# Kernel optimization log

Measured on AMD Instinct MI355X. Metric: run time of the kernel, lower is better.

Reference implementation:

```python
import jax, jax.numpy as jnp
import numpy as np

N_NODES = 50000
N_EDGES = 800000
HIDDEN = 128


def setup_inputs() -> dict:
    key = jax.random.key(0)
    k_emb, k_ei, k1, k2, k3, kb1, kb2, kb3 = jax.random.split(key, 8)
    emb = jax.random.normal(k_emb, (N_NODES, HIDDEN), dtype=jnp.float32)
    edge_index = jax.random.randint(k_ei, (2, N_EDGES), 0, N_NODES, dtype=jnp.int64)
    h = HIDDEN
    # MLP([2h, 4h, h, 1]) weights, Kaiming-uniform-ish init
    def lin(k, fan_in, fan_out):
        bound = 1.0 / np.sqrt(fan_in)
        return jax.random.uniform(k, (fan_in, fan_out), jnp.float32, -bound, bound)
    W1 = lin(k1, 2 * h, 4 * h)
    b1 = jax.random.uniform(kb1, (4 * h,), jnp.float32, -1.0 / np.sqrt(2 * h), 1.0 / np.sqrt(2 * h))
    W2 = lin(k2, 4 * h, h)
    b2 = jax.random.uniform(kb2, (h,), jnp.float32, -1.0 / np.sqrt(4 * h), 1.0 / np.sqrt(4 * h))
    W3 = lin(k3, h, 1)
    b3 = jax.random.uniform(kb3, (1,), jnp.float32, -1.0 / np.sqrt(h), 1.0 / np.sqrt(h))
    return {"emb": emb, "edge_index": edge_index,
            "W1": W1, "b1": b1, "W2": W2, "b2": b2, "W3": W3, "b3": b3}


def reference(emb, edge_index, W1, b1, W2, b2, W3, b3):
    # learn_edge_att=True path: gather endpoints, concat, 3-layer MLP
    col, row = edge_index[0], edge_index[1]
    f12 = jnp.concatenate([emb[col], emb[row]], axis=-1)  # [E, 2h]
    x = jax.nn.relu(f12 @ W1 + b1)                         # [E, 4h]
    x = jax.nn.relu(x @ W2 + b2)                           # [E, h]
    att_log_logits = x @ W3 + b3                           # [E, 1]
    return att_log_logits
```

## Files before the change

### kernel.cpp

```cpp
#include <hip/hip_runtime.h>
#include <hip/hip_bf16.h>
#include <stdint.h>

#define N_EDGES   800000
#define N_NODESC  50000
#define HID       128

typedef __attribute__((ext_vector_type(8))) short bf16x8;
typedef __attribute__((ext_vector_type(4))) short bf16x4;
typedef __attribute__((ext_vector_type(4))) float f32x4;

__device__ __forceinline__ short f2bf(float f) {
    union { float f; uint32_t u; } v; v.f = f;
    uint32_t r = v.u + 0x7FFFu + ((v.u >> 16) & 1u);
    return (short)(r >> 16);
}
__device__ __forceinline__ float bf2f(short s) {
    union { uint32_t u; float f; } v;
    v.u = ((uint32_t)(uint16_t)s) << 16;
    return v.f;
}

#define PQ_OFF   0UL
#define W1S_OFF  102400000UL
#define W2S_OFF  (W1S_OFF + 262144UL)

__global__ __launch_bounds__(256) void swizzle_kernel(const float* __restrict__ W1,
                                                      const float* __restrict__ W2,
                                                      short* __restrict__ W1s,
                                                      short* __restrict__ W2s) {
    int t = blockIdx.x * 256 + threadIdx.x;
    int lane = t & 63;
    int kq = lane >> 4;
    int nn = lane & 15;
    if (t < 16384) {
        int frag = t >> 6;
        int kc = frag >> 6;
        int nt = frag & 63;
        int n = nt * 16 + nn;
        int kbase = kc * 32 + kq * 8;
        bf16x8 v;
        #pragma unroll
        for (int j = 0; j < 8; ++j) {
            int k = kbase + j;
            float f = (n < 512) ? W1[k * 512 + n] : W1[(128 + k) * 512 + (n - 512)];
            v[j] = f2bf(f);
        }
        *(bf16x8*)(W1s + frag * 512 + lane * 8) = v;
    } else if (t < 24576) {
        int t2 = t - 16384;
        int frag = t2 >> 6;
        int kc = frag >> 3;
        int nt = frag & 7;
        int n = nt * 16 + nn;
        int kbase = kc * 32 + kq * 8;
        bf16x8 v;
        #pragma unroll
        for (int j = 0; j < 8; ++j) v[j] = f2bf(W2[(kbase + j) * HID + n]);
        *(bf16x8*)(W2s + frag * 512 + lane * 8) = v;
    }
}

__global__ __launch_bounds__(256) void precompute_kernel(const float* __restrict__ emb,
                                                         const short* __restrict__ W1s,
                                                         const float* __restrict__ b1,
                                                         short* __restrict__ PQ) {
    int lane = threadIdx.x & 63;
    int w = threadIdx.x >> 6;
    int nb = blockIdx.x * 16;
    int m = lane & 15;
    int kq = lane >> 4;

    f32x4 acc[16];
    #pragma unroll
    for (int i = 0; i < 16; ++i) acc[i] = (f32x4){0.f, 0.f, 0.f, 0.f};

    const float* arow = emb + (size_t)(nb + m) * 128 + kq * 8;
    #pragma unroll
    for (int kc = 0; kc < 4; ++kc) {
        f32x4 a0 = *(const f32x4*)(arow + kc * 32);
        f32x4 a1 = *(const f32x4*)(arow + kc * 32 + 4);
        bf16x8 a;
        a[0] = f2bf(a0[0]); a[1] = f2bf(a0[1]); a[2] = f2bf(a0[2]); a[3] = f2bf(a0[3]);
        a[4] = f2bf(a1[0]); a[5] = f2bf(a1[1]); a[6] = f2bf(a1[2]); a[7] = f2bf(a1[3]);
        #pragma unroll
        for (int nt = 0; nt < 16; ++nt) {
            int frag = kc * 64 + (w * 16 + nt);
            bf16x8 b = *(const bf16x8*)(W1s + frag * 512 + lane * 8);
            acc[nt] = __builtin_amdgcn_mfma_f32_16x16x32_bf16(a, b, acc[nt], 0, 0, 0);
        }
    }

    #pragma unroll
    for (int nt = 0; nt < 16; ++nt) {
        int n = w * 256 + nt * 16 + m;
        float bias = (n < 512) ? b1[n] : 0.0f;
        #pragma unroll
        for (int r = 0; r < 4; ++r) {
            int node = nb + kq * 4 + r;
            PQ[(size_t)node * 1024 + n] = f2bf(acc[nt][r] + bias);
        }
    }
}

__global__ __launch_bounds__(256, 2) void edge_kernel(const short* __restrict__ PQ,
                                                      const int* __restrict__ ei,
                                                      const short* __restrict__ W2s,
                                                      const float* __restrict__ b2,
                                                      const float* __restrict__ W3,
                                                      const float* __restrict__ b3,
                                                      float* __restrict__ out) {
    int lane = threadIdx.x & 63;
    int w = threadIdx.x >> 6;
    int e0 = blockIdx.x * 256 + w * 64;
    int m = lane & 15;
    int kq = lane >> 4;

    int idx_c = ei[e0 + lane];
    int idx_r = ei[N_EDGES + e0 + lane];

    const short* pb[4];
    const short* qb[4];
    #pragma unroll
    for (int t = 0; t < 4; ++t) {
        int ce = __shfl(idx_c, t * 16 + m, 64);
        int re = __shfl(idx_r, t * 16 + m, 64);
        pb[t] = PQ + (size_t)ce * 1024 + kq * 8;
        qb[t] = PQ + (size_t)re * 1024 + 512 + kq * 8;
    }

    f32x4 acc[4][8];
    #pragma unroll
    for (int t = 0; t < 4; ++t)
        #pragma unroll
        for (int nt = 0; nt < 8; ++nt) acc[t][nt] = (f32x4){0.f, 0.f, 0.f, 0.f};

    #pragma unroll 1
    for (int kc = 0; kc < 16; ++kc) {
        bf16x8 b[8];
        #pragma unroll
        for (int nt = 0; nt < 8; ++nt)
            b[nt] = *(const bf16x8*)(W2s + (kc * 8 + nt) * 512 + lane * 8);
        #pragma unroll
        for (int t = 0; t < 4; ++t) {
            bf16x8 p = *(const bf16x8*)(pb[t] + kc * 32);
            bf16x8 q = *(const bf16x8*)(qb[t] + kc * 32);
            bf16x8 a;
            #pragma unroll
            for (int j = 0; j < 8; ++j) {
                float f = bf2f(p[j]) + bf2f(q[j]);
                f = f > 0.f ? f : 0.f;
                a[j] = f2bf(f);
            }
            #pragma unroll
            for (int nt = 0; nt < 8; ++nt)
                acc[t][nt] = __builtin_amdgcn_mfma_f32_16x16x32_bf16(a, b[nt], acc[t][nt], 0, 0, 0);
        }
    }

    float b2v[8], w3v[8];
    #pragma unroll
    for (int nt = 0; nt < 8; ++nt) {
        b2v[nt] = b2[nt * 16 + m];
        w3v[nt] = W3[nt * 16 + m];
    }
    float b3s = b3[0];
    #pragma unroll
    for (int t = 0; t < 4; ++t) {
        float partial[4] = {0.f, 0.f, 0.f, 0.f};
        #pragma unroll
        for (int nt = 0; nt < 8; ++nt) {
            #pragma unroll
            for (int r = 0; r < 4; ++r) {
                float x2 = acc[t][nt][r] + b2v[nt];
                x2 = x2 > 0.f ? x2 : 0.f;
                partial[r] += x2 * w3v[nt];
            }
        }
        #pragma unroll
        for (int r = 0; r < 4; ++r) {
            #pragma unroll
            for (int off = 1; off < 16; off <<= 1)
                partial[r] += __shfl_xor(partial[r], off, 64);
            if (m == 0) out[e0 + t * 16 + kq * 4 + r] = partial[r] + b3s;
        }
    }
}

extern "C" void kernel_launch(void* const* d_in, const int* in_sizes, int n_in,
                              void* d_out, int out_size, void* d_ws, size_t ws_size,
                              hipStream_t stream) {
    const float* emb = (const float*)d_in[0];
    const int*   ei  = (const int*)d_in[1];
    const float* W1  = (const float*)d_in[2];
    const float* b1  = (const float*)d_in[3];
    const float* W2  = (const float*)d_in[4];
    const float* b2  = (const float*)d_in[5];
    const float* W3  = (const float*)d_in[6];
    const float* b3  = (const float*)d_in[7];
    float* out = (float*)d_out;

    short* PQ  = (short*)((char*)d_ws + PQ_OFF);
    short* W1s = (short*)((char*)d_ws + W1S_OFF);
    short* W2s = (short*)((char*)d_ws + W2S_OFF);

    swizzle_kernel<<<96, 256, 0, stream>>>(W1, W2, W1s, W2s);
    precompute_kernel<<<N_NODESC / 16, 256, 0, stream>>>(emb, W1s, b1, PQ);
    edge_kernel<<<N_EDGES / 256, 256, 0, stream>>>(PQ, ei, W2s, b2, W3, b3, out);
}
```

Before: 430.6 us.

## Retile edge and precompute kernels, use packed bf16 conversions

The edge kernel now processes 32 edges per wave instead of 64, which halves the accumulator registers. It raises the launch-bounds occupancy hint to 3 and fully unrolls the k loop so gather loads can be issued early. The precompute kernel handles 32 nodes per block, reusing each W1 fragment load for two MFMA tiles, with bounds clamping for the tail. Float-to-bf16 conversion and the add+relu path use packed two-element intrinsics. Smaller edge tiles double the per-edge W2 fragment load traffic, and full unrolling adds register pressure.

```diff
diff --git a/kernel.cpp b/kernel.cpp
--- a/kernel.cpp
+++ b/kernel.cpp
@@ -7,18 +7,38 @@
 #define HID       128
 
 typedef __attribute__((ext_vector_type(8))) short bf16x8;
-typedef __attribute__((ext_vector_type(4))) short bf16x4;
 typedef __attribute__((ext_vector_type(4))) float f32x4;
+typedef __attribute__((ext_vector_type(4))) unsigned int u32x4;
 
 __device__ __forceinline__ short f2bf(float f) {
     union { float f; uint32_t u; } v; v.f = f;
     uint32_t r = v.u + 0x7FFFu + ((v.u >> 16) & 1u);
     return (short)(r >> 16);
 }
-__device__ __forceinline__ float bf2f(short s) {
-    union { uint32_t u; float f; } v;
-    v.u = ((uint32_t)(uint16_t)s) << 16;
-    return v.f;
+
+__device__ __forceinline__ uint32_t packbf2(float lo, float hi) {
+    float2 t; t.x = lo; t.y = hi;
+    __hip_bfloat162 h = __float22bfloat162_rn(t);
+    uint32_t u;
+    __builtin_memcpy(&u, &h, 4);
+    return u;
+}
+
+__device__ __forceinline__ uint32_t addrelu2(uint32_t a, uint32_t b) {
+    union { uint32_t u; float f; } alo, ahi, blo, bhi;
+    alo.u = a << 16;  ahi.u = a & 0xFFFF0000u;
+    blo.u = b << 16;  bhi.u = b & 0xFFFF0000u;
+    float slo = alo.f + blo.f;  slo = slo > 0.f ? slo : 0.f;
+    float shi = ahi.f + bhi.f;  shi = shi > 0.f ? shi : 0.f;
+    return packbf2(slo, shi);
+}
+__device__ __forceinline__ bf16x8 addrelu8(u32x4 p, u32x4 q) {
+    u32x4 r;
+    #pragma unroll
+    for (int j = 0; j < 4; ++j) r[j] = addrelu2(p[j], q[j]);
+    bf16x8 out;
+    __builtin_memcpy(&out, &r, 16);
+    return out;
 }
 
 #define PQ_OFF   0UL
@@ -67,27 +87,41 @@
                                                          short* __restrict__ PQ) {
     int lane = threadIdx.x & 63;
     int w = threadIdx.x >> 6;
-    int nb = blockIdx.x * 16;
+    int nb = blockIdx.x * 32;
     int m = lane & 15;
     int kq = lane >> 4;
 
-    f32x4 acc[16];
-    #pragma unroll
-    for (int i = 0; i < 16; ++i) acc[i] = (f32x4){0.f, 0.f, 0.f, 0.f};
-
-    const float* arow = emb + (size_t)(nb + m) * 128 + kq * 8;
+    int n0 = nb + m;       if (n0 > N_NODESC - 1) n0 = N_NODESC - 1;
+    int n1 = nb + 16 + m;  if (n1 > N_NODESC - 1) n1 = N_NODESC - 1;
+    const float* a0p = emb + (size_t)n0 * 128 + kq * 8;
+    const float* a1p = emb + (size_t)n1 * 128 + kq * 8;
+
+    f32x4 acc[2][16];
+    #pragma unroll
+    for (int mt = 0; mt < 2; ++mt)
+        #pragma unroll
+        for (int i = 0; i < 16; ++i) acc[mt][i] = (f32x4){0.f, 0.f, 0.f, 0.f};
+
     #pragma unroll
     for (int kc = 0; kc < 4; ++kc) {
-        f32x4 a0 = *(const f32x4*)(arow + kc * 32);
-        f32x4 a1 = *(const f32x4*)(arow + kc * 32 + 4);
-        bf16x8 a;
-        a[0] = f2bf(a0[0]); a[1] = f2bf(a0[1]); a[2] = f2bf(a0[2]); a[3] = f2bf(a0[3]);
-        a[4] = f2bf(a1[0]); a[5] = f2bf(a1[1]); a[6] = f2bf(a1[2]); a[7] = f2bf(a1[3]);
+        f32x4 x0 = *(const f32x4*)(a0p + kc * 32);
+        f32x4 x1 = *(const f32x4*)(a0p + kc * 32 + 4);
+        f32x4 y0 = *(const f32x4*)(a1p + kc * 32);
+        f32x4 y1 = *(const f32x4*)(a1p + kc * 32 + 4);
+        u32x4 au, bu;
+        au[0] = packbf2(x0[0], x0[1]); au[1] = packbf2(x0[2], x0[3]);
+        au[2] = packbf2(x1[0], x1[1]); au[3] = packbf2(x1[2], x1[3]);
+        bu[0] = packbf2(y0[0], y0[1]); bu[1] = packbf2(y0[2], y0[3]);
+        bu[2] = packbf2(y1[0], y1[1]); bu[3] = packbf2(y1[2], y1[3]);
+        bf16x8 a0, a1;
+        __builtin_memcpy(&a0, &au, 16);
+        __builtin_memcpy(&a1, &bu, 16);
         #pragma unroll
         for (int nt = 0; nt < 16; ++nt) {
             int frag = kc * 64 + (w * 16 + nt);
             bf16x8 b = *(const bf16x8*)(W1s + frag * 512 + lane * 8);
-            acc[nt] = __builtin_amdgcn_mfma_f32_16x16x32_bf16(a, b, acc[nt], 0, 0, 0);
+            acc[0][nt] = __builtin_amdgcn_mfma_f32_16x16x32_bf16(a0, b, acc[0][nt], 0, 0, 0);
+            acc[1][nt] = __builtin_amdgcn_mfma_f32_16x16x32_bf16(a1, b, acc[1][nt], 0, 0, 0);
         }
     }
 
@@ -96,14 +130,18 @@
         int n = w * 256 + nt * 16 + m;
         float bias = (n < 512) ? b1[n] : 0.0f;
         #pragma unroll
-        for (int r = 0; r < 4; ++r) {
-            int node = nb + kq * 4 + r;
-            PQ[(size_t)node * 1024 + n] = f2bf(acc[nt][r] + bias);
-        }
-    }
-}
-
-__global__ __launch_bounds__(256, 2) void edge_kernel(const short* __restrict__ PQ,
+        for (int mt = 0; mt < 2; ++mt) {
+            #pragma unroll
+            for (int r = 0; r < 4; ++r) {
+                int node = nb + mt * 16 + kq * 4 + r;
+                if (node < N_NODESC)
+                    PQ[(size_t)node * 1024 + n] = f2bf(acc[mt][nt][r] + bias);
+            }
+        }
+    }
+}
+
+__global__ __launch_bounds__(256, 3) void edge_kernel(const short* __restrict__ PQ,
                                                       const int* __restrict__ ei,
                                                       const short* __restrict__ W2s,
                                                       const float* __restrict__ b2,
@@ -112,49 +150,43 @@
                                                       float* __restrict__ out) {
     int lane = threadIdx.x & 63;
     int w = threadIdx.x >> 6;
-    int e0 = blockIdx.x * 256 + w * 64;
+    int e0 = blockIdx.x * 128 + w * 32;
     int m = lane & 15;
     int kq = lane >> 4;
 
-    int idx_c = ei[e0 + lane];
-    int idx_r = ei[N_EDGES + e0 + lane];
-
-    const short* pb[4];
-    const short* qb[4];
-    #pragma unroll
-    for (int t = 0; t < 4; ++t) {
-        int ce = __shfl(idx_c, t * 16 + m, 64);
-        int re = __shfl(idx_r, t * 16 + m, 64);
-        pb[t] = PQ + (size_t)ce * 1024 + kq * 8;
-        qb[t] = PQ + (size_t)re * 1024 + 512 + kq * 8;
-    }
-
-    f32x4 acc[4][8];
-    #pragma unroll
-    for (int t = 0; t < 4; ++t)
+    int ii = (lane < 32) ? ei[e0 + lane] : ei[N_EDGES + e0 + (lane - 32)];
+
+    int c0 = __shfl(ii, m, 64);
+    int c1 = __shfl(ii, 16 + m, 64);
+    int r0 = __shfl(ii, 32 + m, 64);
+    int r1 = __shfl(ii, 48 + m, 64);
+    const short* pb0 = PQ + (size_t)c0 * 1024 + kq * 8;
+    const short* pb1 = PQ + (size_t)c1 * 1024 + kq * 8;
+    const short* qb0 = PQ + (size_t)r0 * 1024 + 512 + kq * 8;
+    const short* qb1 = PQ + (size_t)r1 * 1024 + 512 + kq * 8;
+
+    f32x4 acc[2][8];
+    #pragma unroll
+    for (int t = 0; t < 2; ++t)
         #pragma unroll
         for (int nt = 0; nt < 8; ++nt) acc[t][nt] = (f32x4){0.f, 0.f, 0.f, 0.f};
 
-    #pragma unroll 1
+    #pragma unroll
     for (int kc = 0; kc < 16; ++kc) {
+        u32x4 p0 = *(const u32x4*)(pb0 + kc * 32);
+        u32x4 q0 = *(const u32x4*)(qb0 + kc * 32);
+        u32x4 p1 = *(const u32x4*)(pb1 + kc * 32);
+        u32x4 q1 = *(const u32x4*)(qb1 + kc * 32);
         bf16x8 b[8];
         #pragma unroll
         for (int nt = 0; nt < 8; ++nt)
             b[nt] = *(const bf16x8*)(W2s + (kc * 8 + nt) * 512 + lane * 8);
-        #pragma unroll
-        for (int t = 0; t < 4; ++t) {
-            bf16x8 p = *(const bf16x8*)(pb[t] + kc * 32);
-            bf16x8 q = *(const bf16x8*)(qb[t] + kc * 32);
-            bf16x8 a;
-            #pragma unroll
-            for (int j = 0; j < 8; ++j) {
-                float f = bf2f(p[j]) + bf2f(q[j]);
-                f = f > 0.f ? f : 0.f;
-                a[j] = f2bf(f);
-            }
-            #pragma unroll
-            for (int nt = 0; nt < 8; ++nt)
-                acc[t][nt] = __builtin_amdgcn_mfma_f32_16x16x32_bf16(a, b[nt], acc[t][nt], 0, 0, 0);
+        bf16x8 a0 = addrelu8(p0, q0);
+        bf16x8 a1 = addrelu8(p1, q1);
+        #pragma unroll
+        for (int nt = 0; nt < 8; ++nt) {
+            acc[0][nt] = __builtin_amdgcn_mfma_f32_16x16x32_bf16(a0, b[nt], acc[0][nt], 0, 0, 0);
+            acc[1][nt] = __builtin_amdgcn_mfma_f32_16x16x32_bf16(a1, b[nt], acc[1][nt], 0, 0, 0);
         }
     }
 
@@ -166,7 +198,7 @@
     }
     float b3s = b3[0];
     #pragma unroll
-    for (int t = 0; t < 4; ++t) {
+    for (int t = 0; t < 2; ++t) {
         float partial[4] = {0.f, 0.f, 0.f, 0.f};
         #pragma unroll
         for (int nt = 0; nt < 8; ++nt) {
@@ -205,6 +237,6 @@
     short* W2s = (short*)((char*)d_ws + W2S_OFF);
 
     swizzle_kernel<<<96, 256, 0, stream>>>(W1, W2, W1s, W2s);
-    precompute_kernel<<<N_NODESC / 16, 256, 0, stream>>>(emb, W1s, b1, PQ);
-    edge_kernel<<<N_EDGES / 256, 256, 0, stream>>>(PQ, ei, W2s, b2, W3, b3, out);
-}
+    precompute_kernel<<<(N_NODESC + 31) / 32, 256, 0, stream>>>(emb, W1s, b1, PQ);
+    edge_kernel<<<N_EDGES / 128, 256, 0, stream>>>(PQ, ei, W2s, b2, W3, b3, out);
+}
```

Result: slower. 545.1 us (+26.6%).
